# Kernel tuning notes

Hardware: AMD Instinct MI355X
Metric: run time of the kernel (lower is better)

## Reference

```python
import jax, jax.numpy as jnp
import numpy as np

N_HEAD, D_HEAD, D_MODEL, MAX_LEN = 16, 64, 1024, 64
T, B = 1024, 4
SCALE = 1.0 / D_HEAD ** 0.5


def setup_inputs() -> dict:
    key = jax.random.key(0)
    k1, k2, k3, k4 = jax.random.split(key, 4)
    s = 0.02
    w = jax.random.normal(k1, (T, B, D_MODEL), jnp.float32)
    Wqkv = jax.random.normal(k2, (3 * N_HEAD * D_HEAD, D_MODEL), jnp.float32) * s
    pos_emb = jax.random.normal(k3, (2 * MAX_LEN + 1, D_HEAD), jnp.float32) * s
    Wo = jax.random.normal(k4, (D_MODEL, N_HEAD * D_HEAD), jnp.float32) * s
    i = jnp.arange(T)
    # causal mask, 3D path of the original: [qlen, klen, bsz], True = masked
    attn_mask = jnp.broadcast_to((i[None, :] > i[:, None])[:, :, None], (T, T, B))
    return {"w": w, "attn_mask": attn_mask, "Wqkv": Wqkv, "pos_emb": pos_emb, "Wo": Wo}


def reference(w, attn_mask, Wqkv, pos_emb, Wo):
    qlen, bsz, _ = w.shape
    klen = qlen
    # qkv projection (no bias), chunk into q, k, v
    heads = jnp.einsum('tbd,ed->tbe', w, Wqkv)            # [T, B, 3*H*Dh]
    q, k, v = jnp.split(heads, 3, axis=-1)
    q = q.reshape(qlen, bsz, N_HEAD, D_HEAD).transpose(1, 2, 0, 3) * SCALE  # [B,H,T,Dh]
    k = k.reshape(klen, bsz, N_HEAD, D_HEAD).transpose(1, 2, 0, 3)
    v = v.reshape(klen, bsz, N_HEAD, D_HEAD).transpose(1, 2, 0, 3)
    # learnable relative position embeddings r[q_pos, k_pos, Dh]
    i = jnp.arange(klen)
    rel = jnp.clip(i[None, :] - i[:, None], -MAX_LEN, MAX_LEN) + MAX_LEN   # [T, T]
    r = pos_emb[rel]                                                       # [T, T, Dh]
    # content score + relative-position score (q already scaled)
    qk = jnp.einsum('bhqd,bhkd->bhqk', q, k)
    qr = jnp.einsum('bhqd,qkd->bhqk', q, r)
    score = qk + qr                                                        # [B,H,T,T]
    m = attn_mask.transpose(2, 0, 1)[:, None]                              # [B,1,T,T]
    score = jnp.where(m, -jnp.inf, score)
    attn = jax.nn.softmax(score, axis=-1)                                  # coverage
    # content context + position context
    ctx = jnp.einsum('bhqk,bhkd->bhqd', attn, v) + jnp.einsum('bhqk,qkd->bhqd', attn, r)
    attn_vec = ctx.transpose(0, 2, 1, 3).reshape(bsz, qlen, N_HEAD * D_HEAD)
    out = jnp.einsum('bte,de->btd', attn_vec, Wo)                          # [B,T,D]
    return jnp.swapaxes(out, 0, 1)                                         # [T,B,D]
```

## Files before the change

### kernel.cpp

```cpp
#include <hip/hip_runtime.h>
#include <hip/hip_bf16.h>
#include <math.h>

#define N_HEAD 16
#define D_HEAD 64
#define T_SEQ 1024
#define BATCH 4
#define QSCALE 0.180336879f

typedef float f32x4 __attribute__((ext_vector_type(4)));
typedef short bf16x8 __attribute__((ext_vector_type(8)));
typedef short bf16x4v __attribute__((ext_vector_type(4)));

#define AS1(p) ((const __attribute__((address_space(1))) void*)(p))
#define AS3(p) ((__attribute__((address_space(3))) void*)(p))

__device__ inline bf16x8 ld8(const __hip_bfloat16* p) {
    bf16x4v lo = *(const bf16x4v*)p;
    bf16x4v hi = *(const bf16x4v*)(p + 4);
    return __builtin_shufflevector(lo, hi, 0, 1, 2, 3, 4, 5, 6, 7);
}

__global__ __launch_bounds__(256) void cast_all(
    const float* __restrict__ s0, __hip_bfloat16* __restrict__ d0, int n0,
    const float* __restrict__ s1, __hip_bfloat16* __restrict__ d1, int n1,
    const float* __restrict__ s2, __hip_bfloat16* __restrict__ d2, int n2) {
    int i = (blockIdx.x * 256 + threadIdx.x) * 8;
    const float* src;
    __hip_bfloat16* dst;
    if (i < n0) { src = s0 + i; dst = d0 + i; }
    else if ((i -= n0) < n1) { src = s1 + i; dst = d1 + i; }
    else if ((i -= n1) < n2) { src = s2 + i; dst = d2 + i; }
    else return;
    float4 a = *(const float4*)src;
    float4 b = *(const float4*)(src + 4);
    __hip_bfloat16 t[8];
    t[0] = __float2bfloat16(a.x); t[1] = __float2bfloat16(a.y);
    t[2] = __float2bfloat16(a.z); t[3] = __float2bfloat16(a.w);
    t[4] = __float2bfloat16(b.x); t[5] = __float2bfloat16(b.y);
    t[6] = __float2bfloat16(b.z); t[7] = __float2bfloat16(b.w);
    *(uint4*)dst = *(const uint4*)t;
}

__global__ __launch_bounds__(256) void qkv_gemm_mfma(
    const __hip_bfloat16* __restrict__ A,
    const __hip_bfloat16* __restrict__ B,
    const float* __restrict__ P,
    __hip_bfloat16* __restrict__ Qb, __hip_bfloat16* __restrict__ Kb,
    __hip_bfloat16* __restrict__ Vtb) {
    constexpr int Kd = 1024;
    __shared__ __hip_bfloat16 As[128 * 64];
    __shared__ __hip_bfloat16 Bs[128 * 64];
    const int tid = threadIdx.x;
    const int w = tid >> 6, lane = tid & 63;
    const int lanelo = lane & 15, quad = lane >> 4;
    const int wm = (w >> 1) * 64, wn = (w & 1) * 64;
    const int m0 = blockIdx.y * 128, n0 = blockIdx.x * 128;

    const int sr = lane >> 3;
    const int sc = ((lane & 7) ^ sr) * 8;
    const __hip_bfloat16* Ag = A + (size_t)(m0 + w * 32 + sr) * Kd + sc;
    const __hip_bfloat16* Bg = B + (size_t)(n0 + w * 32 + sr) * Kd + sc;
    __hip_bfloat16* AsW = As + w * 2048;
    __hip_bfloat16* BsW = Bs + w * 2048;

    f32x4 acc[4][4];
#pragma unroll
    for (int i = 0; i < 4; i++)
#pragma unroll
        for (int j = 0; j < 4; j++) acc[i][j] = (f32x4){0.f, 0.f, 0.f, 0.f};

    const int cswz = lanelo & 7;

    for (int k0 = 0; k0 < Kd; k0 += 64) {
        __syncthreads();
#pragma unroll
        for (int i = 0; i < 4; i++) {
            __builtin_amdgcn_global_load_lds(AS1(Ag + k0 + i * 8 * Kd), AS3(AsW + i * 512), 16, 0, 0);
            __builtin_amdgcn_global_load_lds(AS1(Bg + k0 + i * 8 * Kd), AS3(BsW + i * 512), 16, 0, 0);
        }
        __syncthreads();
#pragma unroll
        for (int h = 0; h < 2; h++) {
            const int c16 = (((h * 4 + quad) ^ cswz)) * 8;
            bf16x8 af[4], bfr[4];
#pragma unroll
            for (int i = 0; i < 4; i++)
                af[i] = *(const bf16x8*)(As + (size_t)(wm + i * 16 + lanelo) * 64 + c16);
#pragma unroll
            for (int j = 0; j < 4; j++)
                bfr[j] = *(const bf16x8*)(Bs + (size_t)(wn + j * 16 + lanelo) * 64 + c16);
#pragma unroll
            for (int i = 0; i < 4; i++)
#pragma unroll
                for (int j = 0; j < 4; j++)
                    acc[i][j] = __builtin_amdgcn_mfma_f32_16x16x32_bf16(af[i], bfr[j], acc[i][j], 0, 0, 0);
        }
    }

    const int part = n0 >> 10;
    float p0v[4] = {0.f, 0.f, 0.f, 0.f};
    if (part == 2) {
#pragma unroll
        for (int j = 0; j < 4; j++) p0v[j] = P[j * 16 + lanelo];
    }
#pragma unroll
    for (int i = 0; i < 4; i++)
#pragma unroll
        for (int j = 0; j < 4; j++)
#pragma unroll
            for (int reg = 0; reg < 4; reg++) {
                const int row = m0 + wm + i * 16 + quad * 4 + reg;
                const int col = n0 + wn + j * 16 + lanelo;
                const int t = row >> 2, b = row & 3;
                const int e = col & 1023, h = e >> 6, d = e & 63;
                const float v = acc[i][j][reg];
                if (part == 0)
                    Qb[((size_t)(b * 16 + h) * 1024 + t) * 64 + d] = __float2bfloat16(v * QSCALE);
                else if (part == 1)
                    Kb[((size_t)(b * 16 + h) * 1024 + t) * 64 + d] = __float2bfloat16(v);
                else
                    Vtb[((size_t)(b * 16 + h) * 64 + d) * 1024 + t] = __float2bfloat16(v + p0v[j]);
            }
}

__global__ __launch_bounds__(256) void out_gemm_mfma(
    const __hip_bfloat16* __restrict__ A,
    const __hip_bfloat16* __restrict__ B,
    float* __restrict__ out) {
    constexpr int Kd = 1024;
    __shared__ __hip_bfloat16 As[128 * 64];
    __shared__ __hip_bfloat16 Bs[64 * 64];
    const int tid = threadIdx.x;
    const int w = tid >> 6, lane = tid & 63;
    const int lanelo = lane & 15, quad = lane >> 4;
    const int wm = (w >> 1) * 64, wn = (w & 1) * 32;
    const int m0 = blockIdx.y * 128, n0 = blockIdx.x * 64;

    const int sr = lane >> 3;
    const int sc = ((lane & 7) ^ sr) * 8;
    const __hip_bfloat16* Ag = A + (size_t)(m0 + w * 32 + sr) * Kd + sc;
    const __hip_bfloat16* Bg = B + (size_t)(n0 + w * 16 + sr) * Kd + sc;
    __hip_bfloat16* AsW = As + w * 2048;
    __hip_bfloat16* BsW = Bs + w * 1024;

    f32x4 acc[4][2];
#pragma unroll
    for (int i = 0; i < 4; i++)
#pragma unroll
        for (int j = 0; j < 2; j++) acc[i][j] = (f32x4){0.f, 0.f, 0.f, 0.f};

    const int cswz = lanelo & 7;

    for (int k0 = 0; k0 < Kd; k0 += 64) {
        __syncthreads();
#pragma unroll
        for (int i = 0; i < 4; i++)
            __builtin_amdgcn_global_load_lds(AS1(Ag + k0 + i * 8 * Kd), AS3(AsW + i * 512), 16, 0, 0);
#pragma unroll
        for (int i = 0; i < 2; i++)
            __builtin_amdgcn_global_load_lds(AS1(Bg + k0 + i * 8 * Kd), AS3(BsW + i * 512), 16, 0, 0);
        __syncthreads();
#pragma unroll
        for (int h = 0; h < 2; h++) {
            const int c16 = (((h * 4 + quad) ^ cswz)) * 8;
            bf16x8 af[4], bfr[2];
#pragma unroll
            for (int i = 0; i < 4; i++)
                af[i] = *(const bf16x8*)(As + (size_t)(wm + i * 16 + lanelo) * 64 + c16);
#pragma unroll
            for (int j = 0; j < 2; j++)
                bfr[j] = *(const bf16x8*)(Bs + (size_t)(wn + j * 16 + lanelo) * 64 + c16);
#pragma unroll
            for (int i = 0; i < 4; i++)
#pragma unroll
                for (int j = 0; j < 2; j++)
                    acc[i][j] = __builtin_amdgcn_mfma_f32_16x16x32_bf16(af[i], bfr[j], acc[i][j], 0, 0, 0);
        }
    }

#pragma unroll
    for (int i = 0; i < 4; i++)
#pragma unroll
        for (int j = 0; j < 2; j++)
#pragma unroll
            for (int reg = 0; reg < 4; reg++) {
                const int row = m0 + wm + i * 16 + quad * 4 + reg;
                const int col = n0 + wn + j * 16 + lanelo;
                const int b = row >> 10, t = row & 1023;
                out[(size_t)(t * 4 + b) * 1024 + col] = acc[i][j][reg];
            }
}

__global__ __launch_bounds__(256) void flash_attn(
    const __hip_bfloat16* __restrict__ Qb,
    const __hip_bfloat16* __restrict__ Kb,
    const __hip_bfloat16* __restrict__ Vtb,
    const float* __restrict__ P,
    __hip_bfloat16* __restrict__ av) {
    __shared__ __hip_bfloat16 Ks[64][72];
    __shared__ __hip_bfloat16 Vs[64][72];
    __shared__ __hip_bfloat16 Pl[4][16][68];
    __shared__ __hip_bfloat16 Pband[4][2][16][68];
    __shared__ __hip_bfloat16 QPl[4][2][16][66];

    const int px = blockIdx.x;
    const int TB = 15 - px, TS = px;
    const int bh = blockIdx.y;
    const int b = bh >> 4, h = bh & 15;
    const int tid = threadIdx.x;
    const int w = tid >> 6, lane = tid & 63;
    const int lanelo = lane & 15, quad = lane >> 4;
    const size_t qkbase = (size_t)bh * 1024 * 64;
    const size_t vbase  = (size_t)bh * 64 * 1024;

    const int sr = tid >> 2;
    const int sc = (tid & 3) << 4;
    const __hip_bfloat16* kgb = Kb + qkbase + (size_t)sr * 64 + sc;
    const __hip_bfloat16* vgb = Vtb + vbase + (size_t)sr * 1024 + sc;

    {
        short* pb = (short*)&Pband[w][0][0][0];
        for (int i = lane; i < 2 * 16 * 68; i += 64) pb[i] = 0;
    }

    bf16x8 aqb0, aqb1, aqs0, aqs1;
    {
        const __hip_bfloat16* qrb = Qb + qkbase + (size_t)(TB * 64 + w * 16 + lanelo) * 64;
        aqb0 = *(const bf16x8*)(qrb + quad * 8);
        aqb1 = *(const bf16x8*)(qrb + 32 + quad * 8);
        const __hip_bfloat16* qrs = Qb + qkbase + (size_t)(TS * 64 + w * 16 + lanelo) * 64;
        aqs0 = *(const bf16x8*)(qrs + quad * 8);
        aqs1 = *(const bf16x8*)(qrs + 32 + quad * 8);
    }

#pragma unroll
    for (int jj = 0; jj < 5; jj++) {
        const float* prow = P + (size_t)(jj * 16 + lanelo) * 64 + quad * 8;
        float4 pa = *(const float4*)prow;
        float4 pb = *(const float4*)(prow + 4);
        float4 pc = *(const float4*)(prow + 32);
        float4 pd = *(const float4*)(prow + 36);
        __hip_bfloat16 t0[8], t1[8];
        t0[0] = __float2bfloat16(pa.x); t0[1] = __float2bfloat16(pa.y);
        t0[2] = __float2bfloat16(pa.z); t0[3] = __float2bfloat16(pa.w);
        t0[4] = __float2bfloat16(pb.x); t0[5] = __float2bfloat16(pb.y);
        t0[6] = __float2bfloat16(pb.z); t0[7] = __float2bfloat16(pb.w);
        t1[0] = __float2bfloat16(pc.x); t1[1] = __float2bfloat16(pc.y);
        t1[2] = __float2bfloat16(pc.z); t1[3] = __float2bfloat16(pc.w);
        t1[4] = __float2bfloat16(pd.x); t1[5] = __float2bfloat16(pd.y);
        t1[6] = __float2bfloat16(pd.z); t1[7] = __float2bfloat16(pd.w);
        f32x4 accB = (f32x4){0.f, 0.f, 0.f, 0.f};
        accB = __builtin_amdgcn_mfma_f32_16x16x32_bf16(aqb0, *(const bf16x8*)t0, accB, 0, 0, 0);
        accB = __builtin_amdgcn_mfma_f32_16x16x32_bf16(aqb1, *(const bf16x8*)t1, accB, 0, 0, 0);
        f32x4 accS = (f32x4){0.f, 0.f, 0.f, 0.f};
        accS = __builtin_amdgcn_mfma_f32_16x16x32_bf16(aqs0, *(const bf16x8*)t0, accS, 0, 0, 0);
        accS = __builtin_amdgcn_mfma_f32_16x16x32_bf16(aqs1, *(const bf16x8*)t1, accS, 0, 0, 0);
#pragma unroll
        for (int reg = 0; reg < 4; reg++) {
            QPl[w][0][quad * 4 + reg][jj * 16 + lanelo] = __float2bfloat16(accB[reg]);
            QPl[w][1][quad * 4 + reg][jj * 16 + lanelo] = __float2bfloat16(accS[reg]);
        }
    }
    float qp0b[4], qp0s[4];
#pragma unroll
    for (int reg = 0; reg < 4; reg++) {
        qp0b[reg] = (float)QPl[w][0][quad * 4 + reg][0];
        qp0s[reg] = (float)QPl[w][1][quad * 4 + reg][0];
    }

    f32x4 o_accB[4], o_lB, o_accS[4], o_lS;
#pragma unroll
    for (int dt = 0; dt < 4; dt++) {
        o_accB[dt] = (f32x4){0.f, 0.f, 0.f, 0.f};
        o_accS[dt] = (f32x4){0.f, 0.f, 0.f, 0.f};
    }
    o_lB = (f32x4){0.f, 0.f, 0.f, 0.f};
    o_lS = (f32x4){0.f, 0.f, 0.f, 0.f};
    const short one_bf = 0x3F80;
    const bf16x8 vones = {one_bf, one_bf, one_bf, one_bf, one_bf, one_bf, one_bf, one_bf};

    auto do_qtile = [&](int tq, int Tq, const bf16x8& a0, const bf16x8& a1,
                        const float* qp0, f32x4* o_acc, f32x4& o_l, int kt) {
        f32x4 s_acc[4];
#pragma unroll
        for (int ct = 0; ct < 4; ct++) {
            bf16x8 b0 = *(const bf16x8*)&Ks[ct * 16 + lanelo][quad * 8];
            bf16x8 b1 = *(const bf16x8*)&Ks[ct * 16 + lanelo][32 + quad * 8];
            f32x4 acc = (f32x4){0.f, 0.f, 0.f, 0.f};
            acc = __builtin_amdgcn_mfma_f32_16x16x32_bf16(a0, b0, acc, 0, 0, 0);
            acc = __builtin_amdgcn_mfma_f32_16x16x32_bf16(a1, b1, acc, 0, 0, 0);
            s_acc[ct] = acc;
        }
        const int q0 = Tq * 64 + w * 16;
        const int obase = q0 - kt * 64;
        if (kt < Tq - 1) {
#pragma unroll
            for (int ct = 0; ct < 4; ct++)
#pragma unroll
                for (int reg = 0; reg < 4; reg++) {
                    const float p = __builtin_exp2f(s_acc[ct][reg] + qp0[reg]);
                    Pl[w][quad * 4 + reg][ct * 16 + lanelo] = __float2bfloat16(p);
                }
        } else {
#pragma unroll
            for (int ct = 0; ct < 4; ct++)
#pragma unroll
                for (int reg = 0; reg < 4; reg++) {
                    const int rloc = quad * 4 + reg;
                    const int kl = ct * 16 + lanelo;
                    const int o = obase + rloc - kl;
                    const int idx = (o >= 64 || o < 0) ? 0 : (64 - o);
                    const float add = (float)QPl[w][tq][rloc][idx];
                    const float p = (o < 0) ? 0.f : __builtin_exp2f(s_acc[ct][reg] + add);
                    const __hip_bfloat16 pbv = __float2bfloat16(p);
                    Pl[w][rloc][kl] = pbv;
                    if (o >= 0 && o <= 63) Pband[w][tq][rloc][63 - o] = pbv;
                }
        }
#pragma unroll
        for (int c = 0; c < 2; c++) {
            bf16x8 ap = ld8(&Pl[w][lanelo][c * 32 + quad * 8]);
#pragma unroll
            for (int dt = 0; dt < 4; dt++) {
                bf16x8 bv = *(const bf16x8*)&Vs[dt * 16 + lanelo][c * 32 + quad * 8];
                o_acc[dt] = __builtin_amdgcn_mfma_f32_16x16x32_bf16(ap, bv, o_acc[dt], 0, 0, 0);
            }
            o_l = __builtin_amdgcn_mfma_f32_16x16x32_bf16(ap, vones, o_l, 0, 0, 0);
        }
    };

    uint4 rk0, rk1, rv0, rv1;
    rk0 = *(const uint4*)(kgb);
    rk1 = *(const uint4*)(kgb + 8);
    rv0 = *(const uint4*)(vgb);
    rv1 = *(const uint4*)(vgb + 8);

    for (int kt = 0; kt <= TB; kt++) {
        __syncthreads();
        *(uint4*)&Ks[sr][sc]     = rk0;
        *(uint4*)&Ks[sr][sc + 8] = rk1;
        *(uint4*)&Vs[sr][sc]     = rv0;
        *(uint4*)&Vs[sr][sc + 8] = rv1;
        if (kt < TB) {
            const __hip_bfloat16* kg = kgb + (size_t)(kt + 1) * 4096;
            const __hip_bfloat16* vg = vgb + (size_t)(kt + 1) * 64;
            rk0 = *(const uint4*)(kg);
            rk1 = *(const uint4*)(kg + 8);
            rv0 = *(const uint4*)(vg);
            rv1 = *(const uint4*)(vg + 8);
        }
        __syncthreads();

        do_qtile(0, TB, aqb0, aqb1, qp0b, o_accB, o_lB, kt);
        if (kt <= TS) do_qtile(1, TS, aqs0, aqs1, qp0s, o_accS, o_lS, kt);
    }

#pragma unroll
    for (int tq = 0; tq < 2; tq++) {
        f32x4* o_acc = tq == 0 ? o_accB : o_accS;
        f32x4& o_l   = tq == 0 ? o_lB : o_lS;
        const int q0 = (tq == 0 ? TB : TS) * 64 + w * 16;
#pragma unroll
        for (int c = 0; c < 2; c++) {
            bf16x8 ab = ld8(&Pband[w][tq][lanelo][c * 32 + quad * 8]);
#pragma unroll
            for (int dt = 0; dt < 4; dt++) {
                const int d = dt * 16 + lanelo;
                const float p0 = P[d];
                __hip_bfloat16 tb[8];
#pragma unroll
                for (int jj = 0; jj < 8; jj++) {
                    const int kk = c * 32 + quad * 8 + jj;
                    tb[jj] = __float2bfloat16(P[(kk + 1) * 64 + d] - p0);
                }
                o_acc[dt] = __builtin_amdgcn_mfma_f32_16x16x32_bf16(ab, *(const bf16x8*)tb, o_acc[dt], 0, 0, 0);
            }
        }
        float rinv[4];
#pragma unroll
        for (int reg = 0; reg < 4; reg++) rinv[reg] = 1.0f / o_l[reg];
#pragma unroll
        for (int dt = 0; dt < 4; dt++) {
            const int cdim = dt * 16 + lanelo;
#pragma unroll
            for (int reg = 0; reg < 4; reg++) {
                const int q = q0 + quad * 4 + reg;
                av[((size_t)(b * 1024 + q)) * 1024 + h * 64 + cdim] =
                    __float2bfloat16(o_acc[dt][reg] * rinv[reg]);
            }
        }
    }
}

extern "C" void kernel_launch(void* const* d_in, const int* in_sizes, int n_in,
                              void* d_out, int out_size, void* d_ws, size_t ws_size,
                              hipStream_t stream) {
    const float* w       = (const float*)d_in[0];
    const float* Wqkv    = (const float*)d_in[2];
    const float* pos_emb = (const float*)d_in[3];
    const float* Wo      = (const float*)d_in[4];
    float* out = (float*)d_out;

    const size_t SZ = (size_t)BATCH * N_HEAD * T_SEQ * D_HEAD;
    __hip_bfloat16* wb     = (__hip_bfloat16*)d_ws;
    __hip_bfloat16* Wqkvb  = wb + SZ;
    __hip_bfloat16* Wob    = Wqkvb + 3 * 1024 * 1024;
    __hip_bfloat16* Qb     = Wob + 1024 * 1024;
    __hip_bfloat16* Kb     = Qb + SZ;
    __hip_bfloat16* Vtb    = Kb + SZ;
    __hip_bfloat16* AVb    = Vtb + SZ;

    const int n_w = 4096 * 1024, n_wqkv = 3072 * 1024, n_wo = 1024 * 1024;
    const int n_tot = n_w + n_wqkv + n_wo;
    cast_all<<<n_tot / 2048, 256, 0, stream>>>(w, wb, n_w, Wqkv, Wqkvb, n_wqkv, Wo, Wob, n_wo);

    qkv_gemm_mfma<<<dim3(3072 / 128, 4096 / 128), 256, 0, stream>>>(wb, Wqkvb, pos_emb, Qb, Kb, Vtb);
    flash_attn<<<dim3(8, 64), 256, 0, stream>>>(Qb, Kb, Vtb, pos_emb, AVb);
    out_gemm_mfma<<<dim3(1024 / 64, 4096 / 128), 256, 0, stream>>>(AVb, Wob, out);
}
```

Measured before the change: 200.0 us.

## Fuse fp32-to-bf16 casts into QKV GEMM loads and attention prologue

```diff
diff --git a/kernel.cpp b/kernel.cpp
--- a/kernel.cpp
+++ b/kernel.cpp
@@ -21,36 +21,26 @@
     return __builtin_shufflevector(lo, hi, 0, 1, 2, 3, 4, 5, 6, 7);
 }
 
-__global__ __launch_bounds__(256) void cast_all(
-    const float* __restrict__ s0, __hip_bfloat16* __restrict__ d0, int n0,
-    const float* __restrict__ s1, __hip_bfloat16* __restrict__ d1, int n1,
-    const float* __restrict__ s2, __hip_bfloat16* __restrict__ d2, int n2) {
-    int i = (blockIdx.x * 256 + threadIdx.x) * 8;
-    const float* src;
-    __hip_bfloat16* dst;
-    if (i < n0) { src = s0 + i; dst = d0 + i; }
-    else if ((i -= n0) < n1) { src = s1 + i; dst = d1 + i; }
-    else if ((i -= n1) < n2) { src = s2 + i; dst = d2 + i; }
-    else return;
-    float4 a = *(const float4*)src;
-    float4 b = *(const float4*)(src + 4);
+__device__ inline bf16x8 cvt_frag(const float* rowp, int quad, int key) {
+    float4 lo = *(const float4*)(rowp + (size_t)(((2 * quad) ^ key) * 4));
+    float4 hi = *(const float4*)(rowp + (size_t)(((2 * quad + 1) ^ key) * 4));
     __hip_bfloat16 t[8];
-    t[0] = __float2bfloat16(a.x); t[1] = __float2bfloat16(a.y);
-    t[2] = __float2bfloat16(a.z); t[3] = __float2bfloat16(a.w);
-    t[4] = __float2bfloat16(b.x); t[5] = __float2bfloat16(b.y);
-    t[6] = __float2bfloat16(b.z); t[7] = __float2bfloat16(b.w);
-    *(uint4*)dst = *(const uint4*)t;
-}
-
-__global__ __launch_bounds__(256) void qkv_gemm_mfma(
-    const __hip_bfloat16* __restrict__ A,
-    const __hip_bfloat16* __restrict__ B,
+    t[0] = __float2bfloat16(lo.x); t[1] = __float2bfloat16(lo.y);
+    t[2] = __float2bfloat16(lo.z); t[3] = __float2bfloat16(lo.w);
+    t[4] = __float2bfloat16(hi.x); t[5] = __float2bfloat16(hi.y);
+    t[6] = __float2bfloat16(hi.z); t[7] = __float2bfloat16(hi.w);
+    return *(const bf16x8*)t;
+}
+
+__global__ __launch_bounds__(256) void qkv_gemm_f32(
+    const float* __restrict__ A,
+    const float* __restrict__ B,
     const float* __restrict__ P,
     __hip_bfloat16* __restrict__ Qb, __hip_bfloat16* __restrict__ Kb,
     __hip_bfloat16* __restrict__ Vtb) {
     constexpr int Kd = 1024;
-    __shared__ __hip_bfloat16 As[128 * 64];
-    __shared__ __hip_bfloat16 Bs[128 * 64];
+    __shared__ float As[128 * 32];
+    __shared__ float Bs[128 * 32];
     const int tid = threadIdx.x;
     const int w = tid >> 6, lane = tid & 63;
     const int lanelo = lane & 15, quad = lane >> 4;
@@ -58,11 +48,11 @@
     const int m0 = blockIdx.y * 128, n0 = blockIdx.x * 128;
 
     const int sr = lane >> 3;
-    const int sc = ((lane & 7) ^ sr) * 8;
-    const __hip_bfloat16* Ag = A + (size_t)(m0 + w * 32 + sr) * Kd + sc;
-    const __hip_bfloat16* Bg = B + (size_t)(n0 + w * 32 + sr) * Kd + sc;
-    __hip_bfloat16* AsW = As + w * 2048;
-    __hip_bfloat16* BsW = Bs + w * 2048;
+    const int su = (lane & 7) ^ sr;
+    const float* Ag = A + (size_t)(m0 + w * 32 + sr) * Kd + su * 4;
+    const float* Bg = B + (size_t)(n0 + w * 32 + sr) * Kd + su * 4;
+    float* AsW = As + (size_t)(w * 32) * 32;
+    float* BsW = Bs + (size_t)(w * 32) * 32;
 
     f32x4 acc[4][4];
 #pragma unroll
@@ -70,32 +60,28 @@
 #pragma unroll
         for (int j = 0; j < 4; j++) acc[i][j] = (f32x4){0.f, 0.f, 0.f, 0.f};
 
-    const int cswz = lanelo & 7;
-
-    for (int k0 = 0; k0 < Kd; k0 += 64) {
+    const int keyA = lanelo & 7;
+
+    for (int k0 = 0; k0 < Kd; k0 += 32) {
         __syncthreads();
 #pragma unroll
         for (int i = 0; i < 4; i++) {
-            __builtin_amdgcn_global_load_lds(AS1(Ag + k0 + i * 8 * Kd), AS3(AsW + i * 512), 16, 0, 0);
-            __builtin_amdgcn_global_load_lds(AS1(Bg + k0 + i * 8 * Kd), AS3(BsW + i * 512), 16, 0, 0);
-        }
-        __syncthreads();
-#pragma unroll
-        for (int h = 0; h < 2; h++) {
-            const int c16 = (((h * 4 + quad) ^ cswz)) * 8;
-            bf16x8 af[4], bfr[4];
-#pragma unroll
-            for (int i = 0; i < 4; i++)
-                af[i] = *(const bf16x8*)(As + (size_t)(wm + i * 16 + lanelo) * 64 + c16);
+            __builtin_amdgcn_global_load_lds(AS1(Ag + k0 + (size_t)i * 8 * Kd), AS3(AsW + i * 256), 16, 0, 0);
+            __builtin_amdgcn_global_load_lds(AS1(Bg + k0 + (size_t)i * 8 * Kd), AS3(BsW + i * 256), 16, 0, 0);
+        }
+        __syncthreads();
+        bf16x8 af[4], bfr[4];
+#pragma unroll
+        for (int i = 0; i < 4; i++)
+            af[i] = cvt_frag(As + (size_t)(wm + i * 16 + lanelo) * 32, quad, keyA);
+#pragma unroll
+        for (int j = 0; j < 4; j++)
+            bfr[j] = cvt_frag(Bs + (size_t)(wn + j * 16 + lanelo) * 32, quad, keyA);
+#pragma unroll
+        for (int i = 0; i < 4; i++)
 #pragma unroll
             for (int j = 0; j < 4; j++)
-                bfr[j] = *(const bf16x8*)(Bs + (size_t)(wn + j * 16 + lanelo) * 64 + c16);
-#pragma unroll
-            for (int i = 0; i < 4; i++)
-#pragma unroll
-                for (int j = 0; j < 4; j++)
-                    acc[i][j] = __builtin_amdgcn_mfma_f32_16x16x32_bf16(af[i], bfr[j], acc[i][j], 0, 0, 0);
-        }
+                acc[i][j] = __builtin_amdgcn_mfma_f32_16x16x32_bf16(af[i], bfr[j], acc[i][j], 0, 0, 0);
     }
 
     const int part = n0 >> 10;
@@ -197,6 +183,8 @@
     const __hip_bfloat16* __restrict__ Kb,
     const __hip_bfloat16* __restrict__ Vtb,
     const float* __restrict__ P,
+    const float* __restrict__ Wo,
+    __hip_bfloat16* __restrict__ Wob,
     __hip_bfloat16* __restrict__ av) {
     __shared__ __hip_bfloat16 Ks[64][72];
     __shared__ __hip_bfloat16 Vs[64][72];
@@ -209,6 +197,19 @@
     const int bh = blockIdx.y;
     const int b = bh >> 4, h = bh & 15;
     const int tid = threadIdx.x;
+
+    {
+        const int gid = (bh * 8 + px) * 256 + tid;
+        const float4 a = *(const float4*)(Wo + (size_t)gid * 8);
+        const float4 c = *(const float4*)(Wo + (size_t)gid * 8 + 4);
+        __hip_bfloat16 t[8];
+        t[0] = __float2bfloat16(a.x); t[1] = __float2bfloat16(a.y);
+        t[2] = __float2bfloat16(a.z); t[3] = __float2bfloat16(a.w);
+        t[4] = __float2bfloat16(c.x); t[5] = __float2bfloat16(c.y);
+        t[6] = __float2bfloat16(c.z); t[7] = __float2bfloat16(c.w);
+        *(uint4*)(Wob + (size_t)gid * 8) = *(const uint4*)t;
+    }
+
     const int w = tid >> 6, lane = tid & 63;
     const int lanelo = lane & 15, quad = lane >> 4;
     const size_t qkbase = (size_t)bh * 1024 * 64;
@@ -411,11 +412,7 @@
     __hip_bfloat16* Vtb    = Kb + SZ;
     __hip_bfloat16* AVb    = Vtb + SZ;
 
-    const int n_w = 4096 * 1024, n_wqkv = 3072 * 1024, n_wo = 1024 * 1024;
-    const int n_tot = n_w + n_wqkv + n_wo;
-    cast_all<<<n_tot / 2048, 256, 0, stream>>>(w, wb, n_w, Wqkv, Wqkvb, n_wqkv, Wo, Wob, n_wo);
-
-    qkv_gemm_mfma<<<dim3(3072 / 128, 4096 / 128), 256, 0, stream>>>(wb, Wqkvb, pos_emb, Qb, Kb, Vtb);
-    flash_attn<<<dim3(8, 64), 256, 0, stream>>>(Qb, Kb, Vtb, pos_emb, AVb);
+    qkv_gemm_f32<<<dim3(3072 / 128, 4096 / 128), 256, 0, stream>>>(w, Wqkv, pos_emb, Qb, Kb, Vtb);
+    flash_attn<<<dim3(8, 64), 256, 0, stream>>>(Qb, Kb, Vtb, pos_emb, Wo, Wob, AVb);
     out_gemm_mfma<<<dim3(1024 / 64, 4096 / 128), 256, 0, stream>>>(AVb, Wob, out);
 }
```

Result: no change. 202.4 us (+1.2%).
